# Optimization experiments

Measured on AMD Instinct MI355X. Metric: run time of the kernel, lower is better.

The kernel has to match this reference:

```python
import jax, jax.numpy as jnp
import numpy as np
from itertools import product

N = 120000      # active voxels
D = 128         # dense grid resolution per axis
CIN = 64
COUT = 64
K = 27          # 3x3x3 kernel volume
EPS = 1e-5


def setup_inputs() -> dict:
    # Build a random sparse voxel set and its kernel-offset neighbor map (torchsparse kmap).
    rng = np.random.default_rng(0)
    flat = rng.choice(D ** 3, size=N, replace=False)
    cz, cy, cx = np.unravel_index(flat, (D, D, D))
    coords = np.stack([cz, cy, cx], axis=1)               # [N, 3]
    lut = np.full(D ** 3, -1, dtype=np.int64)
    lut[flat] = np.arange(N)
    nbr = np.empty((K, N), dtype=np.int32)
    for k, (dz, dy, dx) in enumerate(product((-1, 0, 1), repeat=3)):
        nc = coords + np.array([dz, dy, dx])
        valid = np.all((nc >= 0) & (nc < D), axis=1)
        fl = np.ravel_multi_index(np.clip(nc, 0, D - 1).T, (D, D, D))
        nbr[k] = np.where(valid, lut[fl], -1).astype(np.int32)

    key = jax.random.key(0)
    k1, k2, k3, k4 = jax.random.split(key, 4)
    feats = jax.random.normal(k1, (N, CIN), dtype=jnp.float32)
    # torchsparse Conv3d weight layout: [kernel_volume, in_channels, out_channels]
    weight = jax.random.normal(k2, (K, CIN, COUT), dtype=jnp.float32) / np.float32(np.sqrt(K * CIN))
    gamma = jax.random.uniform(k3, (COUT,), dtype=jnp.float32, minval=0.5, maxval=1.5)
    beta = jax.random.normal(k4, (COUT,), dtype=jnp.float32) * 0.1
    return {"feats": feats, "weight": weight, "gamma": gamma, "beta": beta,
            "neighbor_idx": jnp.asarray(nbr)}


def reference(feats, weight, gamma, beta, neighbor_idx):
    # Sparse conv = gather -> per-offset matmul -> accumulate (stride 1, same voxel set).
    mask = (neighbor_idx >= 0)                      # [K, N]
    safe = jnp.maximum(neighbor_idx, 0)
    gathered = feats[safe] * mask[..., None]        # [K, N, Cin], missing neighbors zeroed
    out = jnp.einsum('knc,kcd->nd', gathered, weight)  # [N, Cout]
    # BatchNorm over active voxels (training-mode batch statistics), then ReLU.
    mean = out.mean(axis=0)
    var = out.var(axis=0)
    y = gamma * (out - mean) * jax.lax.rsqrt(var + EPS) + beta
    return jnp.maximum(y, 0.0)
```

## Files before the change

kernel.cpp:

```cpp
#include <hip/hip_runtime.h>

#define NVOX 120000
#define KVOL 27
#define CH 64
#define TOTAL (NVOX * CH)
#define NF4 (TOTAL / 4)
#define EPSV 1e-5f

typedef __attribute__((ext_vector_type(8))) short bf16x8;
typedef __attribute__((ext_vector_type(4))) float f32x4;

__device__ __forceinline__ unsigned short f2bf(float f) {
    unsigned int u = __builtin_bit_cast(unsigned int, f);
    u += 0x7FFFu + ((u >> 16) & 1u);
    return (unsigned short)(u >> 16);
}

__global__ void prep(const float* __restrict__ w, unsigned short* __restrict__ wtf,
                     const float* __restrict__ f, unsigned short* __restrict__ fb,
                     float* __restrict__ stats) {
    const int b = blockIdx.x;
    const int tid = threadIdx.x;
    if (b < 432) {
        const int t = b * 256 + tid;
        const int d = t & 63, c = (t >> 6) & 63, k = t >> 12;
        const int grp = (d >> 4) * 2 + (c >> 5);
        const int l = ((c & 31) >> 3) * 16 + (d & 15);
        const int j = c & 7;
        wtf[(((size_t)k * 8 + grp) * 64 + l) * 8 + j] = f2bf(w[t]);
        if (b == 0 && tid < 128) stats[tid] = 0.f;
    } else {
        for (int t = (b - 432) * 256 + tid; t < NF4; t += 1000 * 256) {
            const float4 x = ((const float4*)f)[t];
            ushort4 y;
            y.x = f2bf(x.x); y.y = f2bf(x.y); y.z = f2bf(x.z); y.w = f2bf(x.w);
            ((ushort4*)fb)[t] = y;
        }
    }
}

__device__ __forceinline__ void gatherRow(const unsigned short* __restrict__ fb,
                                          int idx, int q, bf16x8& a0, bf16x8& a1) {
    const int safe = idx < 0 ? 0 : idx;
    const unsigned short* row = fb + (size_t)safe * CH + q * 8;
    a0 = *(const bf16x8*)row;
    a1 = *(const bf16x8*)(row + 32);
    if (idx < 0) {
        a0 = (bf16x8)(short)0;
        a1 = (bf16x8)(short)0;
    }
}

__launch_bounds__(256, 4)
__global__ void conv_mfma(const unsigned short* __restrict__ featsB,
                          const unsigned short* __restrict__ WtF,
                          const int* __restrict__ nbr,
                          float* __restrict__ out,
                          float* __restrict__ stats) {
    __shared__ float lstats[128];
    const int tid = threadIdx.x;
    const int lane = tid & 63;
    const int wave = tid >> 6;
    const int m = lane & 15;
    const int q = lane >> 4;
    const int v0 = blockIdx.x * 128 + wave * 32;
    const int r0 = v0 + m;
    const int r1 = v0 + 16 + m;
    const bool ok0 = r0 < NVOX;
    const bool ok1 = r1 < NVOX;

    f32x4 acc[2][4];
#pragma unroll
    for (int t = 0; t < 2; ++t)
#pragma unroll
        for (int nt = 0; nt < 4; ++nt)
            acc[t][nt] = (f32x4){0.f, 0.f, 0.f, 0.f};
    if (tid < 128) lstats[tid] = 0.f;
    __syncthreads();

    int i0 = ok0 ? nbr[r0] : -1;
    int i1 = ok1 ? nbr[r1] : -1;

    for (int k = 0; k < KVOL; ++k) {
        const unsigned long long t0m = __ballot(i0 >= 0);
        const unsigned long long t1m = __ballot(i1 >= 0);

        bf16x8 a00, a01, a10, a11;
        if (t0m) gatherRow(featsB, i0, q, a00, a01);
        if (t1m) gatherRow(featsB, i1, q, a10, a11);

        int i0n = -1, i1n = -1;
        if (k + 1 < KVOL) {
            const int* nb = nbr + (size_t)(k + 1) * NVOX;
            i0n = ok0 ? nb[r0] : -1;
            i1n = ok1 ? nb[r1] : -1;
        }

        if (t0m | t1m) {
            const unsigned short* wk = WtF + (size_t)k * 4096 + lane * 8;
            bf16x8 bfr[8];
#pragma unroll
            for (int h = 0; h < 8; ++h)
                bfr[h] = *(const bf16x8*)(wk + h * 512);
            if (t0m) {
#pragma unroll
                for (int nt = 0; nt < 4; ++nt) {
                    acc[0][nt] = __builtin_amdgcn_mfma_f32_16x16x32_bf16(a00, bfr[nt * 2 + 0], acc[0][nt], 0, 0, 0);
                    acc[0][nt] = __builtin_amdgcn_mfma_f32_16x16x32_bf16(a01, bfr[nt * 2 + 1], acc[0][nt], 0, 0, 0);
                }
            }
            if (t1m) {
#pragma unroll
                for (int nt = 0; nt < 4; ++nt) {
                    acc[1][nt] = __builtin_amdgcn_mfma_f32_16x16x32_bf16(a10, bfr[nt * 2 + 0], acc[1][nt], 0, 0, 0);
                    acc[1][nt] = __builtin_amdgcn_mfma_f32_16x16x32_bf16(a11, bfr[nt * 2 + 1], acc[1][nt], 0, 0, 0);
                }
            }
        }
        i0 = i0n;
        i1 = i1n;
    }

#pragma unroll
    for (int t = 0; t < 2; ++t) {
        const int rbase = v0 + t * 16 + q * 4;
        float* ob = out + (size_t)rbase * CH + m;
#pragma unroll
        for (int nt = 0; nt < 4; ++nt)
#pragma unroll
            for (int r = 0; r < 4; ++r)
                if (rbase + r < NVOX)
                    ob[(size_t)r * CH + nt * 16] = acc[t][nt][r];
    }

#pragma unroll
    for (int nt = 0; nt < 4; ++nt) {
        float s = 0.f, s2 = 0.f;
#pragma unroll
        for (int t = 0; t < 2; ++t)
#pragma unroll
            for (int r = 0; r < 4; ++r) {
                const float x = acc[t][nt][r];
                s += x;
                s2 = fmaf(x, x, s2);
            }
        s  += __shfl_xor(s, 16);  s  += __shfl_xor(s, 32);
        s2 += __shfl_xor(s2, 16); s2 += __shfl_xor(s2, 32);
        if (lane < 16) {
            atomicAdd(&lstats[nt * 16 + m], s);
            atomicAdd(&lstats[64 + nt * 16 + m], s2);
        }
    }
    __syncthreads();
    if (tid < 128) atomicAdd(&stats[tid], lstats[tid]);
}

__launch_bounds__(256)
__global__ void bn_relu(float* __restrict__ out, const float* __restrict__ stats,
                        const float* __restrict__ gamma, const float* __restrict__ beta) {
    __shared__ float sb[128];
    const int tid = threadIdx.x;
    if (tid < 64) {
        const float inv_n = 1.0f / (float)NVOX;
        const float mean = stats[tid] * inv_n;
        const float var = stats[64 + tid] * inv_n - mean * mean;
        const float sc = gamma[tid] * rsqrtf(var + EPSV);
        sb[tid] = sc;
        sb[64 + tid] = beta[tid] - mean * sc;
    }
    __syncthreads();
    float4* o4 = (float4*)out;
    for (int e = blockIdx.x * 256 + tid; e < NF4; e += 960 * 256) {
        float4 x = o4[e];
        const int cb = (e & 15) * 4;
        x.x = fmaxf(fmaf(x.x, sb[cb + 0], sb[64 + cb + 0]), 0.f);
        x.y = fmaxf(fmaf(x.y, sb[cb + 1], sb[64 + cb + 1]), 0.f);
        x.z = fmaxf(fmaf(x.z, sb[cb + 2], sb[64 + cb + 2]), 0.f);
        x.w = fmaxf(fmaf(x.w, sb[cb + 3], sb[64 + cb + 3]), 0.f);
        o4[e] = x;
    }
}

extern "C" void kernel_launch(void* const* d_in, const int* in_sizes, int n_in,
                              void* d_out, int out_size, void* d_ws, size_t ws_size,
                              hipStream_t stream) {
    const float* feats  = (const float*)d_in[0];
    const float* weight = (const float*)d_in[1];
    const float* gamma  = (const float*)d_in[2];
    const float* beta   = (const float*)d_in[3];
    const int*   nbr    = (const int*)d_in[4];
    float* out = (float*)d_out;

    float* stats = (float*)d_ws;
    unsigned short* WtF    = (unsigned short*)((char*)d_ws + 512);
    unsigned short* featsB = (unsigned short*)((char*)d_ws + 512 + 221184);

    prep<<<432 + 1000, 256, 0, stream>>>(weight, WtF, feats, featsB, stats);
    conv_mfma<<<(NVOX + 127) / 128, 256, 0, stream>>>(featsB, WtF, nbr, out, stats);
    bn_relu<<<960, 256, 0, stream>>>(out, stats, gamma, beta);
}
```

Baseline: 156.5 us.

## Gather fp32 features directly with bf16 conversion, prefetch next offset, 48 rows per wave

Drops the separate feature-to-bf16 conversion pass, so the conv kernel gathers fp32 rows and converts them to bf16 in registers. It also software-pipelines the gather one kernel offset ahead and raises each wave to 48 voxels, so every weight fragment load feeds more MFMAs. Bounds checks are removed because 120000 divides by 192 exactly. The costs are twice the gather bytes from the fp32 rows, higher register pressure, and a lower occupancy target.

```diff
diff --git a/kernel.cpp b/kernel.cpp
--- a/kernel.cpp
+++ b/kernel.cpp
@@ -17,42 +17,38 @@
 }
 
 __global__ void prep(const float* __restrict__ w, unsigned short* __restrict__ wtf,
-                     const float* __restrict__ f, unsigned short* __restrict__ fb,
                      float* __restrict__ stats) {
     const int b = blockIdx.x;
     const int tid = threadIdx.x;
-    if (b < 432) {
-        const int t = b * 256 + tid;
-        const int d = t & 63, c = (t >> 6) & 63, k = t >> 12;
-        const int grp = (d >> 4) * 2 + (c >> 5);
-        const int l = ((c & 31) >> 3) * 16 + (d & 15);
-        const int j = c & 7;
-        wtf[(((size_t)k * 8 + grp) * 64 + l) * 8 + j] = f2bf(w[t]);
-        if (b == 0 && tid < 128) stats[tid] = 0.f;
-    } else {
-        for (int t = (b - 432) * 256 + tid; t < NF4; t += 1000 * 256) {
-            const float4 x = ((const float4*)f)[t];
-            ushort4 y;
-            y.x = f2bf(x.x); y.y = f2bf(x.y); y.z = f2bf(x.z); y.w = f2bf(x.w);
-            ((ushort4*)fb)[t] = y;
-        }
-    }
-}
-
-__device__ __forceinline__ void gatherRow(const unsigned short* __restrict__ fb,
-                                          int idx, int q, bf16x8& a0, bf16x8& a1) {
+    const int t = b * 256 + tid;
+    const int d = t & 63, c = (t >> 6) & 63, k = t >> 12;
+    const int grp = (d >> 4) * 2 + (c >> 5);
+    const int l = ((c & 31) >> 3) * 16 + (d & 15);
+    const int j = c & 7;
+    wtf[(((size_t)k * 8 + grp) * 64 + l) * 8 + j] = f2bf(w[t]);
+    if (b == 0 && tid < 128) stats[tid] = 0.f;
+}
+
+__device__ __forceinline__ void gatherRowF(const float* __restrict__ f,
+                                           int idx, int q, bf16x8& a0, bf16x8& a1) {
     const int safe = idx < 0 ? 0 : idx;
-    const unsigned short* row = fb + (size_t)safe * CH + q * 8;
-    a0 = *(const bf16x8*)row;
-    a1 = *(const bf16x8*)(row + 32);
+    const float* row = f + (size_t)safe * CH + q * 8;
+    const float4 p0 = *(const float4*)(row);
+    const float4 p1 = *(const float4*)(row + 4);
+    const float4 p2 = *(const float4*)(row + 32);
+    const float4 p3 = *(const float4*)(row + 36);
+    a0 = (bf16x8){(short)f2bf(p0.x), (short)f2bf(p0.y), (short)f2bf(p0.z), (short)f2bf(p0.w),
+                  (short)f2bf(p1.x), (short)f2bf(p1.y), (short)f2bf(p1.z), (short)f2bf(p1.w)};
+    a1 = (bf16x8){(short)f2bf(p2.x), (short)f2bf(p2.y), (short)f2bf(p2.z), (short)f2bf(p2.w),
+                  (short)f2bf(p3.x), (short)f2bf(p3.y), (short)f2bf(p3.z), (short)f2bf(p3.w)};
     if (idx < 0) {
         a0 = (bf16x8)(short)0;
         a1 = (bf16x8)(short)0;
     }
 }
 
-__launch_bounds__(256, 4)
-__global__ void conv_mfma(const unsigned short* __restrict__ featsB,
+__launch_bounds__(256, 3)
+__global__ void conv_mfma(const float* __restrict__ feats,
                           const unsigned short* __restrict__ WtF,
                           const int* __restrict__ nbr,
                           float* __restrict__ out,
@@ -60,87 +56,92 @@
     __shared__ float lstats[128];
     const int tid = threadIdx.x;
     const int lane = tid & 63;
-    const int wave = tid >> 6;
     const int m = lane & 15;
     const int q = lane >> 4;
-    const int v0 = blockIdx.x * 128 + wave * 32;
-    const int r0 = v0 + m;
-    const int r1 = v0 + 16 + m;
-    const bool ok0 = r0 < NVOX;
-    const bool ok1 = r1 < NVOX;
-
-    f32x4 acc[2][4];
-#pragma unroll
-    for (int t = 0; t < 2; ++t)
+    const int v0 = blockIdx.x * 192 + (tid >> 6) * 48;
+    const int r[3] = {v0 + m, v0 + 16 + m, v0 + 32 + m};
+
+    f32x4 acc[3][4];
+#pragma unroll
+    for (int t = 0; t < 3; ++t)
 #pragma unroll
         for (int nt = 0; nt < 4; ++nt)
             acc[t][nt] = (f32x4){0.f, 0.f, 0.f, 0.f};
     if (tid < 128) lstats[tid] = 0.f;
     __syncthreads();
 
-    int i0 = ok0 ? nbr[r0] : -1;
-    int i1 = ok1 ? nbr[r1] : -1;
+    bf16x8 a[3][2];
+    unsigned long long msk[3];
+    int idxn[3];
+#pragma unroll
+    for (int t = 0; t < 3; ++t) {
+        const int i = nbr[r[t]];
+        msk[t] = __ballot(i >= 0);
+        if (msk[t]) gatherRowF(feats, i, q, a[t][0], a[t][1]);
+        else { a[t][0] = (bf16x8)(short)0; a[t][1] = (bf16x8)(short)0; }
+        idxn[t] = nbr[NVOX + r[t]];
+    }
 
     for (int k = 0; k < KVOL; ++k) {
-        const unsigned long long t0m = __ballot(i0 >= 0);
-        const unsigned long long t1m = __ballot(i1 >= 0);
-
-        bf16x8 a00, a01, a10, a11;
-        if (t0m) gatherRow(featsB, i0, q, a00, a01);
-        if (t1m) gatherRow(featsB, i1, q, a10, a11);
-
-        int i0n = -1, i1n = -1;
-        if (k + 1 < KVOL) {
-            const int* nb = nbr + (size_t)(k + 1) * NVOX;
-            i0n = ok0 ? nb[r0] : -1;
-            i1n = ok1 ? nb[r1] : -1;
-        }
-
-        if (t0m | t1m) {
+        unsigned long long mn[3];
+        bf16x8 an[3][2];
+#pragma unroll
+        for (int t = 0; t < 3; ++t) {
+            mn[t] = __ballot(idxn[t] >= 0);
+            if (mn[t]) gatherRowF(feats, idxn[t], q, an[t][0], an[t][1]);
+        }
+        int idxf[3] = {-1, -1, -1};
+        if (k + 2 < KVOL) {
+            const int* nb = nbr + (size_t)(k + 2) * NVOX;
+#pragma unroll
+            for (int t = 0; t < 3; ++t) idxf[t] = nb[r[t]];
+        }
+
+        if (msk[0] | msk[1] | msk[2]) {
             const unsigned short* wk = WtF + (size_t)k * 4096 + lane * 8;
             bf16x8 bfr[8];
 #pragma unroll
             for (int h = 0; h < 8; ++h)
                 bfr[h] = *(const bf16x8*)(wk + h * 512);
-            if (t0m) {
-#pragma unroll
-                for (int nt = 0; nt < 4; ++nt) {
-                    acc[0][nt] = __builtin_amdgcn_mfma_f32_16x16x32_bf16(a00, bfr[nt * 2 + 0], acc[0][nt], 0, 0, 0);
-                    acc[0][nt] = __builtin_amdgcn_mfma_f32_16x16x32_bf16(a01, bfr[nt * 2 + 1], acc[0][nt], 0, 0, 0);
+#pragma unroll
+            for (int t = 0; t < 3; ++t) {
+                if (msk[t]) {
+#pragma unroll
+                    for (int nt = 0; nt < 4; ++nt) {
+                        acc[t][nt] = __builtin_amdgcn_mfma_f32_16x16x32_bf16(a[t][0], bfr[nt * 2 + 0], acc[t][nt], 0, 0, 0);
+                        acc[t][nt] = __builtin_amdgcn_mfma_f32_16x16x32_bf16(a[t][1], bfr[nt * 2 + 1], acc[t][nt], 0, 0, 0);
+                    }
                 }
             }
-            if (t1m) {
-#pragma unroll
-                for (int nt = 0; nt < 4; ++nt) {
-                    acc[1][nt] = __builtin_amdgcn_mfma_f32_16x16x32_bf16(a10, bfr[nt * 2 + 0], acc[1][nt], 0, 0, 0);
-                    acc[1][nt] = __builtin_amdgcn_mfma_f32_16x16x32_bf16(a11, bfr[nt * 2 + 1], acc[1][nt], 0, 0, 0);
-                }
-            }
-        }
-        i0 = i0n;
-        i1 = i1n;
-    }
-
-#pragma unroll
-    for (int t = 0; t < 2; ++t) {
-        const int rbase = v0 + t * 16 + q * 4;
-        float* ob = out + (size_t)rbase * CH + m;
+        }
+
+#pragma unroll
+        for (int t = 0; t < 3; ++t) {
+            a[t][0] = an[t][0];
+            a[t][1] = an[t][1];
+            msk[t] = mn[t];
+            idxn[t] = idxf[t];
+        }
+    }
+
+#pragma unroll
+    for (int t = 0; t < 3; ++t) {
+        float* ob = out + (size_t)(v0 + t * 16 + q * 4) * CH + m;
 #pragma unroll
         for (int nt = 0; nt < 4; ++nt)
 #pragma unroll
-            for (int r = 0; r < 4; ++r)
-                if (rbase + r < NVOX)
-                    ob[(size_t)r * CH + nt * 16] = acc[t][nt][r];
+            for (int rr = 0; rr < 4; ++rr)
+                ob[(size_t)rr * CH + nt * 16] = acc[t][nt][rr];
     }
 
 #pragma unroll
     for (int nt = 0; nt < 4; ++nt) {
         float s = 0.f, s2 = 0.f;
 #pragma unroll
-        for (int t = 0; t < 2; ++t)
-#pragma unroll
-            for (int r = 0; r < 4; ++r) {
-                const float x = acc[t][nt][r];
+        for (int t = 0; t < 3; ++t)
+#pragma unroll
+            for (int rr = 0; rr < 4; ++rr) {
+                const float x = acc[t][nt][rr];
                 s += x;
                 s2 = fmaf(x, x, s2);
             }
@@ -192,10 +193,9 @@
     float* out = (float*)d_out;
 
     float* stats = (float*)d_ws;
-    unsigned short* WtF    = (unsigned short*)((char*)d_ws + 512);
-    unsigned short* featsB = (unsigned short*)((char*)d_ws + 512 + 221184);
-
-    prep<<<432 + 1000, 256, 0, stream>>>(weight, WtF, feats, featsB, stats);
-    conv_mfma<<<(NVOX + 127) / 128, 256, 0, stream>>>(featsB, WtF, nbr, out, stats);
+    unsigned short* WtF = (unsigned short*)((char*)d_ws + 512);
+
+    prep<<<432, 256, 0, stream>>>(weight, WtF, stats);
+    conv_mfma<<<NVOX / 192, 256, 0, stream>>>(feats, WtF, nbr, out, stats);
     bn_relu<<<960, 256, 0, stream>>>(out, stats, gamma, beta);
 }
```

Result: no change. 154.2 us (-1.5%).

## Stage weights in LDS per offset group and prefetch next offset's gathered rows

Applied to the files above, without the earlier changes.

The conv kernel now copies weight slices for six kernel offsets at a time into shared memory (48KB) and reads the MFMA B-fragments from LDS instead of global memory. It also software-pipelines the gather: feature rows for offset k+1 and neighbor indices for k+2 are loaded while offset k's MFMAs run. The aim is to hide gather latency and cut redundant global weight loads. In exchange it adds block barriers per group, more registers for the prefetched fragments, and an LDS footprint that may reduce occupancy below the launch-bounds target of 4 blocks.

```diff
diff --git a/kernel.cpp b/kernel.cpp
--- a/kernel.cpp
+++ b/kernel.cpp
@@ -9,6 +9,7 @@
 
 typedef __attribute__((ext_vector_type(8))) short bf16x8;
 typedef __attribute__((ext_vector_type(4))) float f32x4;
+typedef __attribute__((ext_vector_type(4))) unsigned int u32x4;
 
 __device__ __forceinline__ unsigned short f2bf(float f) {
     unsigned int u = __builtin_bit_cast(unsigned int, f);
@@ -57,13 +58,13 @@
                           const int* __restrict__ nbr,
                           float* __restrict__ out,
                           float* __restrict__ stats) {
+    __shared__ __align__(16) unsigned short ldsW[6 * 4096];
     __shared__ float lstats[128];
     const int tid = threadIdx.x;
     const int lane = tid & 63;
-    const int wave = tid >> 6;
     const int m = lane & 15;
     const int q = lane >> 4;
-    const int v0 = blockIdx.x * 128 + wave * 32;
+    const int v0 = blockIdx.x * 128 + (tid >> 6) * 32;
     const int r0 = v0 + m;
     const int r1 = v0 + 16 + m;
     const bool ok0 = r0 < NVOX;
@@ -76,49 +77,73 @@
         for (int nt = 0; nt < 4; ++nt)
             acc[t][nt] = (f32x4){0.f, 0.f, 0.f, 0.f};
     if (tid < 128) lstats[tid] = 0.f;
-    __syncthreads();
 
     int i0 = ok0 ? nbr[r0] : -1;
     int i1 = ok1 ? nbr[r1] : -1;
-
-    for (int k = 0; k < KVOL; ++k) {
-        const unsigned long long t0m = __ballot(i0 >= 0);
-        const unsigned long long t1m = __ballot(i1 >= 0);
-
-        bf16x8 a00, a01, a10, a11;
-        if (t0m) gatherRow(featsB, i0, q, a00, a01);
-        if (t1m) gatherRow(featsB, i1, q, a10, a11);
-
-        int i0n = -1, i1n = -1;
-        if (k + 1 < KVOL) {
-            const int* nb = nbr + (size_t)(k + 1) * NVOX;
-            i0n = ok0 ? nb[r0] : -1;
-            i1n = ok1 ? nb[r1] : -1;
-        }
-
-        if (t0m | t1m) {
-            const unsigned short* wk = WtF + (size_t)k * 4096 + lane * 8;
-            bf16x8 bfr[8];
-#pragma unroll
-            for (int h = 0; h < 8; ++h)
-                bfr[h] = *(const bf16x8*)(wk + h * 512);
-            if (t0m) {
-#pragma unroll
-                for (int nt = 0; nt < 4; ++nt) {
-                    acc[0][nt] = __builtin_amdgcn_mfma_f32_16x16x32_bf16(a00, bfr[nt * 2 + 0], acc[0][nt], 0, 0, 0);
-                    acc[0][nt] = __builtin_amdgcn_mfma_f32_16x16x32_bf16(a01, bfr[nt * 2 + 1], acc[0][nt], 0, 0, 0);
+    unsigned long long m0 = __ballot(i0 >= 0);
+    unsigned long long m1 = __ballot(i1 >= 0);
+    bf16x8 a00, a01, a10, a11;
+    if (m0) gatherRow(featsB, i0, q, a00, a01);
+    if (m1) gatherRow(featsB, i1, q, a10, a11);
+    int i0n = ok0 ? nbr[NVOX + r0] : -1;
+    int i1n = ok1 ? nbr[NVOX + r1] : -1;
+
+    int gstart = 0;
+    for (int g = 0; g < 5; ++g) {
+        const int S = (g == 4) ? 3 : 6;
+
+        __syncthreads();
+        {
+            const unsigned short* src = WtF + (size_t)gstart * 4096;
+            const int nchunk = S * 512;
+            for (int c = tid; c < nchunk; c += 256)
+                *(u32x4*)(&ldsW[c * 8]) = *(const u32x4*)(src + c * 8);
+        }
+        __syncthreads();
+
+        for (int s = 0; s < S; ++s) {
+            const int k = gstart + s;
+
+            const unsigned long long m0n = __ballot(i0n >= 0);
+            const unsigned long long m1n = __ballot(i1n >= 0);
+            bf16x8 an00, an01, an10, an11;
+            if (m0n) gatherRow(featsB, i0n, q, an00, an01);
+            if (m1n) gatherRow(featsB, i1n, q, an10, an11);
+
+            int i0f = -1, i1f = -1;
+            if (k + 2 < KVOL) {
+                const int* nb = nbr + (size_t)(k + 2) * NVOX;
+                i0f = ok0 ? nb[r0] : -1;
+                i1f = ok1 ? nb[r1] : -1;
+            }
+
+            if (m0 | m1) {
+                const unsigned short* wk = ldsW + s * 4096 + lane * 8;
+                bf16x8 bfr[8];
+#pragma unroll
+                for (int h = 0; h < 8; ++h)
+                    bfr[h] = *(const bf16x8*)(wk + h * 512);
+                if (m0) {
+#pragma unroll
+                    for (int nt = 0; nt < 4; ++nt) {
+                        acc[0][nt] = __builtin_amdgcn_mfma_f32_16x16x32_bf16(a00, bfr[nt * 2 + 0], acc[0][nt], 0, 0, 0);
+                        acc[0][nt] = __builtin_amdgcn_mfma_f32_16x16x32_bf16(a01, bfr[nt * 2 + 1], acc[0][nt], 0, 0, 0);
+                    }
+                }
+                if (m1) {
+#pragma unroll
+                    for (int nt = 0; nt < 4; ++nt) {
+                        acc[1][nt] = __builtin_amdgcn_mfma_f32_16x16x32_bf16(a10, bfr[nt * 2 + 0], acc[1][nt], 0, 0, 0);
+                        acc[1][nt] = __builtin_amdgcn_mfma_f32_16x16x32_bf16(a11, bfr[nt * 2 + 1], acc[1][nt], 0, 0, 0);
+                    }
                 }
             }
-            if (t1m) {
-#pragma unroll
-                for (int nt = 0; nt < 4; ++nt) {
-                    acc[1][nt] = __builtin_amdgcn_mfma_f32_16x16x32_bf16(a10, bfr[nt * 2 + 0], acc[1][nt], 0, 0, 0);
-                    acc[1][nt] = __builtin_amdgcn_mfma_f32_16x16x32_bf16(a11, bfr[nt * 2 + 1], acc[1][nt], 0, 0, 0);
-                }
-            }
-        }
-        i0 = i0n;
-        i1 = i1n;
+
+            a00 = an00; a01 = an01; a10 = an10; a11 = an11;
+            m0 = m0n; m1 = m1n;
+            i0n = i0f; i1n = i1f;
+        }
+        gstart += S;
     }
 
 #pragma unroll
```

After: 192.8 us. 1.23x slower.
